# Optimization experiments

Measured on AMD Instinct MI355X. Metric: run time of the kernel, lower is better.

The kernel has to match this reference:

```python
import jax, jax.numpy as jnp
import numpy as np

N = 100000     # total points
PBS = 500      # point_batch_size (hard-coded in module)
K = 100        # num_neighbors
KP = 15        # num_kernel_points
EPS = 1e-5


def _bn(x, g, b, axes):
    # torch BatchNorm in training mode: batch stats, biased variance
    m = jnp.mean(x, axis=axes, keepdims=True)
    v = jnp.var(x, axis=axes, keepdims=True)
    return (x - m) / jnp.sqrt(v + EPS) * g + b


def setup_inputs() -> dict:
    key = jax.random.key(0)
    ks = jax.random.split(key, 16)
    rn = lambda k, sh, s=1.0: jax.random.normal(k, sh, jnp.float32) * s
    return {
        "pts": rn(ks[0], (N, 3)),
        "normal": rn(ks[1], (N, 3)),
        "kp_points": rn(ks[2], (KP, 3)),
        "kp_weights": rn(ks[3], (KP, 3, 128), 0.3),
        "kp_sigma": jnp.float32(1.0),
        "conv1_w": rn(ks[4], (1024, 128), 128 ** -0.5),
        "conv1_b": rn(ks[5], (1024,), 0.02),
        "bn1_g": jnp.ones((1024,), jnp.float32),
        "bn1_b": jnp.zeros((1024,), jnp.float32),
        "fc1_w": rn(ks[6], (512, 1024), 1024 ** -0.5),
        "fc1_b": rn(ks[7], (512,), 0.02),
        "bn4_g": jnp.ones((512,), jnp.float32),
        "bn4_b": jnp.zeros((512,), jnp.float32),
        "fc2_w": rn(ks[8], (256, 512), 512 ** -0.5),
        "fc2_b": rn(ks[9], (256,), 0.02),
        "bn5_g": jnp.ones((256,), jnp.float32),
        "bn5_b": jnp.zeros((256,), jnp.float32),
        "fc3_w": rn(ks[10], (3, 256), 256 ** -0.5),
        "fc3_b": rn(ks[11], (3,), 0.02),
        "index": jax.random.randint(ks[12], (PBS,), 0, N, jnp.int32),
    }


def reference(pts, normal, kp_points, kp_weights, kp_sigma,
              conv1_w, conv1_b, bn1_g, bn1_b,
              fc1_w, fc1_b, bn4_g, bn4_b,
              fc2_w, fc2_b, bn5_g, bn5_b,
              fc3_w, fc3_b, index):
    sel = pts[index]                                               # [B,3]
    # L-inf pairwise distance and kNN (topk of -dist, as in the torch code)
    dist = jnp.max(jnp.abs(sel[:, None, :] - pts[None, :, :]), axis=-1)  # [B,N]
    _, nbr = jax.lax.top_k(-dist, K)                               # [B,K]
    rel = pts[nbr] - sel[:, None, :]                               # [B,K,3]

    # KPConv: gaussian weights vs kernel points, per-kernel-point linear map
    d2 = jnp.sum((rel[:, :, None, :] - kp_points[None, None]) ** 2, axis=-1)  # [B,K,KP]
    w = jnp.exp(-0.5 * d2 / (kp_sigma ** 2))
    wf = rel[:, :, None, :] * w[..., None]                         # [B,K,KP,3]
    h = jax.nn.relu(jnp.einsum('bnkc,kco->bno', wf, kp_weights))   # [B,K,128]

    # 1x1 conv 128->1024, relu then BN over (batch, points) per channel
    h = jnp.einsum('bnc,oc->bno', h, conv1_w) + conv1_b            # [B,K,1024]
    h = _bn(jax.nn.relu(h), bn1_g, bn1_b, (0, 1))
    feat = jnp.max(h, axis=1)                                      # [B,1024]

    feat = _bn(jax.nn.relu(feat @ fc1_w.T + fc1_b), bn4_g, bn4_b, (0,))
    feat = _bn(jax.nn.relu(feat @ fc2_w.T + fc2_b), bn5_g, bn5_b, (0,))
    feat = feat @ fc3_w.T + fc3_b                                  # [B,3]
    return feat, normal[index]
```

## Files before the change

### kernel.cpp

```cpp
#include <hip/hip_runtime.h>
#include <hip/hip_fp16.h>

#define NPTS 100000
#define NB 500
#define KNN 100
#define KPN 15
#define C1 128
#define C2 1024
#define C3 512
#define C4 256

#define G 64
#define NCELLS (G * G * G)
#define GB 5.0f
#define GINVH ((float)G / (2.f * GB))
#define CAND_CAP 2048

typedef _Float16 half8 __attribute__((ext_vector_type(8)));
typedef float f32x4 __attribute__((ext_vector_type(4)));

__device__ __forceinline__ int cell_coord(float x) {
  int c = (int)floorf((x + GB) * GINVH);
  return min(max(c, 0), G - 1);
}
__device__ __forceinline__ int cell_of(float x, float y, float z) {
  return (cell_coord(x) << 12) | (cell_coord(y) << 6) | cell_coord(z);
}

__global__ __launch_bounds__(256) void prep_kernel(
    const float* __restrict__ pts, const float* __restrict__ normal,
    const int* __restrict__ index, const float* __restrict__ w1,
    const float* __restrict__ kpw, const float* __restrict__ fc1w,
    float* __restrict__ sel, float* __restrict__ out2,
    __half* __restrict__ wh, __half* __restrict__ kpwT_hi,
    __half* __restrict__ kpwT_lo, __half* __restrict__ fwhi,
    __half* __restrict__ fwlo, unsigned* __restrict__ cnt) {
  int i = blockIdx.x * 256 + threadIdx.x;
  if (i < NB) {
    int ix = index[i];
    sel[i * 3 + 0] = pts[3 * ix + 0];
    sel[i * 3 + 1] = pts[3 * ix + 1];
    sel[i * 3 + 2] = pts[3 * ix + 2];
    out2[i * 3 + 0] = normal[3 * ix + 0];
    out2[i * 3 + 1] = normal[3 * ix + 1];
    out2[i * 3 + 2] = normal[3 * ix + 2];
  }
  if (i < C2 * C1) wh[i] = __float2half(w1[i]);
  if (i < 128 * 64) {
    int o = i >> 6, j = i & 63;
    float v = (j < 45) ? kpw[j * 128 + o] : 0.f;
    __half hi = __float2half_rn(v);
    kpwT_hi[i] = hi;
    kpwT_lo[i] = __float2half_rn(v - __half2float(hi));
  }
  if (i < C3 * C2) {
    float v = fc1w[i];
    __half hi = __float2half_rn(v);
    fwhi[i] = hi;
    fwlo[i] = __float2half_rn(v - __half2float(hi));
  }
  if (i < NPTS)
    atomicAdd(&cnt[cell_of(pts[3 * i], pts[3 * i + 1], pts[3 * i + 2])], 1u);
}

__global__ __launch_bounds__(256) void grid_scan1_kernel(
    const unsigned* __restrict__ cnt, unsigned* __restrict__ cursor,
    unsigned* __restrict__ chunktot) {
  const int tid = threadIdx.x;
  int base = blockIdx.x * 1024 + tid * 4;
  unsigned c0 = cnt[base], c1 = cnt[base + 1], c2 = cnt[base + 2],
           c3 = cnt[base + 3];
  unsigned tot = c0 + c1 + c2 + c3;
  __shared__ unsigned sb[256];
  sb[tid] = tot;
  __syncthreads();
  for (int off = 1; off < 256; off <<= 1) {
    unsigned add = (tid >= off) ? sb[tid - off] : 0u;
    __syncthreads();
    sb[tid] += add;
    __syncthreads();
  }
  unsigned excl = sb[tid] - tot;
  cursor[base] = excl;
  cursor[base + 1] = excl + c0;
  cursor[base + 2] = excl + c0 + c1;
  cursor[base + 3] = excl + c0 + c1 + c2;
  if (tid == 255) chunktot[blockIdx.x] = sb[255];
}

__global__ __launch_bounds__(256) void grid_scan2_kernel(
    const unsigned* __restrict__ chunktot, unsigned* __restrict__ chunkoff) {
  const int tid = threadIdx.x;
  unsigned v = chunktot[tid];
  __shared__ unsigned sb[256];
  sb[tid] = v;
  __syncthreads();
  for (int off = 1; off < 256; off <<= 1) {
    unsigned add = (tid >= off) ? sb[tid - off] : 0u;
    __syncthreads();
    sb[tid] += add;
    __syncthreads();
  }
  chunkoff[tid] = sb[tid] - v;
}

__global__ __launch_bounds__(256) void grid_scan3_kernel(
    unsigned* __restrict__ cursor, const unsigned* __restrict__ chunkoff) {
  unsigned off = chunkoff[blockIdx.x];
  int base = blockIdx.x * 1024 + threadIdx.x * 4;
#pragma unroll
  for (int j = 0; j < 4; ++j) cursor[base + j] += off;
}

__global__ __launch_bounds__(256) void grid_scatter_kernel(
    const float* __restrict__ pts, unsigned* __restrict__ cursor,
    float4* __restrict__ sorted) {
  int i = blockIdx.x * 256 + threadIdx.x;
  if (i >= NPTS) return;
  float x = pts[3 * i], y = pts[3 * i + 1], z = pts[3 * i + 2];
  unsigned pos = atomicAdd(&cursor[cell_of(x, y, z)], 1u);
  sorted[pos] = make_float4(x, y, z, __int_as_float(i));
}

__device__ __forceinline__ unsigned linf_bits(float px, float py, float pz,
                                              float sx, float sy, float sz) {
  float dx = fabsf(px - sx), dy = fabsf(py - sy), dz = fabsf(pz - sz);
  return __float_as_uint(fmaxf(fmaxf(dx, dy), dz));
}

__global__ __launch_bounds__(256) void knn_kernel(
    const float4* __restrict__ sorted, const unsigned* __restrict__ cnt,
    const unsigned* __restrict__ cursor,
    const float* __restrict__ sel, int* __restrict__ nbr) {
  const int b = blockIdx.x;
  const int tid = threadIdx.x;
  __shared__ unsigned cbits[CAND_CAP];
  __shared__ int cidx[CAND_CAP];
  __shared__ unsigned hist[4096];
  __shared__ unsigned scanbuf[256];
  __shared__ int s_total, s_m, s_mc, s_chunk;
  __shared__ unsigned s_excl, s_bub;

  const float qx = sel[b * 3 + 0], qy = sel[b * 3 + 1], qz = sel[b * 3 + 2];
  const int qcx = cell_coord(qx), qcy = cell_coord(qy), qcz = cell_coord(qz);

  if (tid == 0) s_total = 0;
  __syncthreads();
  int s = 1;
  int pxlo = 1, pxhi = 0, pylo = 1, pyhi = 0, pzlo = 1, pzhi = 0;
  int xlo, xhi, ylo, yhi, zlo, zhi;
  for (;;) {
    xlo = max(qcx - s, 0); xhi = min(qcx + s, G - 1);
    ylo = max(qcy - s, 0); yhi = min(qcy + s, G - 1);
    zlo = max(qcz - s, 0); zhi = min(qcz + s, G - 1);
    int nx = xhi - xlo + 1, ny = yhi - ylo + 1, nz = zhi - zlo + 1;
    int ncell = nx * ny * nz;
    unsigned local = 0;
    for (int ci = tid; ci < ncell; ci += 256) {
      int cz = ci % nz;
      int r = ci / nz;
      int cy = r % ny;
      int cx = r / ny;
      int ax = xlo + cx, ay = ylo + cy, az = zlo + cz;
      if (ax >= pxlo && ax <= pxhi && ay >= pylo && ay <= pyhi &&
          az >= pzlo && az <= pzhi)
        continue;
      local += cnt[(ax << 12) | (ay << 6) | az];
    }
#pragma unroll
    for (int off = 32; off; off >>= 1) local += __shfl_down(local, off);
    if ((tid & 63) == 0) atomicAdd(&s_total, (int)local);
    __syncthreads();
    if (s_total >= KNN || (xlo == 0 && ylo == 0 && zlo == 0 && xhi == G - 1 &&
                           yhi == G - 1 && zhi == G - 1))
      break;
    pxlo = xlo; pxhi = xhi; pylo = ylo; pyhi = yhi; pzlo = zlo; pzhi = zhi;
    ++s;
    __syncthreads();
  }

  if (tid == 0) s_m = 0;
  __syncthreads();
  {
    int nx = xhi - xlo + 1, ny = yhi - ylo + 1, nz = zhi - zlo + 1;
    int ncell = nx * ny * nz;
    for (int ci = tid; ci < ncell; ci += 256) {
      int cz = ci % nz;
      int r = ci / nz;
      int cy = r % ny;
      int cx = r / ny;
      int cell = ((xlo + cx) << 12) | ((ylo + cy) << 6) | (zlo + cz);
      unsigned end = cursor[cell];
      unsigned beg = end - cnt[cell];
      int k = (int)(end - beg);
      if (k > 0) {
        int e0 = atomicAdd(&s_m, k);
        for (unsigned p = beg; p < end; ++p, ++e0) {
          if (e0 < CAND_CAP) {
            float4 f = sorted[p];
            cbits[e0] = linf_bits(f.x, f.y, f.z, qx, qy, qz);
            cidx[e0] = __float_as_int(f.w);
          }
        }
      }
    }
  }
  __syncthreads();
  int m = s_m < CAND_CAP ? s_m : CAND_CAP;

  for (int j = tid; j < 4096; j += 256) hist[j] = 0;
  __syncthreads();
  for (int e = tid; e < m; e += 256) atomicAdd(&hist[cbits[e] >> 19], 1u);
  __syncthreads();
  unsigned csum = 0;
  {
    int c0 = tid * 16;
#pragma unroll
    for (int j = 0; j < 16; ++j) csum += hist[c0 + j];
  }
  scanbuf[tid] = csum;
  __syncthreads();
  for (int off = 1; off < 256; off <<= 1) {
    unsigned add = (tid >= off) ? scanbuf[tid - off] : 0u;
    __syncthreads();
    scanbuf[tid] += add;
    __syncthreads();
  }
  {
    unsigned incl = scanbuf[tid], excl = incl - csum;
    if (excl < KNN && KNN <= incl) {
      s_chunk = tid;
      s_excl = excl;
    }
  }
  __syncthreads();
  if (tid == 0) {
    unsigned cum = s_excl;
    int bin = s_chunk * 16;
    while (cum + hist[bin] < KNN) {
      cum += hist[bin];
      ++bin;
    }
    s_bub = (unsigned)(bin + 1) << 19;
  }
  __syncthreads();

  const unsigned bub = s_bub;
  const float dub = __uint_as_float(bub);
  if (tid == 0) s_mc = 0;
  __syncthreads();
  {
    int xlo2 = min(max((int)floorf((qx - dub + GB) * GINVH), 0), G - 1);
    int xhi2 = min(max((int)floorf((qx + dub + GB) * GINVH), 0), G - 1);
    int ylo2 = min(max((int)floorf((qy - dub + GB) * GINVH), 0), G - 1);
    int yhi2 = min(max((int)floorf((qy + dub + GB) * GINVH), 0), G - 1);
    int zlo2 = min(max((int)floorf((qz - dub + GB) * GINVH), 0), G - 1);
    int zhi2 = min(max((int)floorf((qz + dub + GB) * GINVH), 0), G - 1);
    int nx = xhi2 - xlo2 + 1, ny = yhi2 - ylo2 + 1, nz = zhi2 - zlo2 + 1;
    int ncell = nx * ny * nz;
    for (int ci = tid; ci < ncell; ci += 256) {
      int cz = ci % nz;
      int r = ci / nz;
      int cy = r % ny;
      int cx = r / ny;
      int cell = ((xlo2 + cx) << 12) | ((ylo2 + cy) << 6) | (zlo2 + cz);
      unsigned end = cursor[cell];
      unsigned beg = end - cnt[cell];
      for (unsigned p = beg; p < end; ++p) {
        float4 f = sorted[p];
        unsigned bits = linf_bits(f.x, f.y, f.z, qx, qy, qz);
        if (bits < bub) {
          int e = atomicAdd(&s_mc, 1);
          if (e < CAND_CAP) {
            cbits[e] = bits;
            cidx[e] = __float_as_int(f.w);
          }
        }
      }
    }
  }
  __syncthreads();
  int mc = s_mc < CAND_CAP ? s_mc : CAND_CAP;

  for (int c = tid; c < mc; c += 256) {
    unsigned bc = cbits[c];
    int ic = cidx[c];
    int rank = 0;
    for (int j = 0; j < mc; ++j) {
      unsigned bj = cbits[j];
      rank += (bj < bc || (bj == bc && cidx[j] < ic)) ? 1 : 0;
    }
    if (rank < KNN) nbr[b * KNN + rank] = ic;
  }
}

__global__ __launch_bounds__(512, 2) void kpconv_conv1_kernel(
    const float* __restrict__ pts, const float* __restrict__ sel,
    const int* __restrict__ nbr, const float* __restrict__ kp_points,
    const __half* __restrict__ kpwT_hi, const __half* __restrict__ kpwT_lo,
    const float* __restrict__ kp_sigma, const __half* __restrict__ wh,
    const float* __restrict__ bias, float* __restrict__ featmax,
    float* __restrict__ featmin, float* __restrict__ bnsum,
    float* __restrict__ bnsq) {
  const int b = blockIdx.x;
  const int tid = threadIdx.x;
  const int wave = tid >> 6, lane = tid & 63;
  const int lr = lane & 15, quad = lane >> 4;

  __shared__ __align__(16) char smem[71168];
  __half* As_hi = (__half*)smem;
  __half* As_lo = As_hi + 112 * 72;
  __half* Bs_hi = As_lo + 112 * 72;
  __half* Bs_lo = Bs_hi + 128 * 72;
  float* rel = (float*)(Bs_lo + 128 * 72);
  float* kpp = rel + 100 * 4;
  __half* Hs = (__half*)smem;

  for (int i = tid; i < 128 * 8; i += 512) {
    int row = i >> 3, seg = i & 7;
    *(float4*)&Bs_hi[row * 72 + seg * 8] =
        *(const float4*)&kpwT_hi[row * 64 + seg * 8];
    *(float4*)&Bs_lo[row * 72 + seg * 8] =
        *(const float4*)&kpwT_lo[row * 64 + seg * 8];
  }
  {
    float4 z = make_float4(0.f, 0.f, 0.f, 0.f);
    for (int i = tid; i < 112 * 8; i += 512) {
      int row = i >> 3, seg = i & 7;
      *(float4*)&As_hi[row * 72 + seg * 8] = z;
      *(float4*)&As_lo[row * 72 + seg * 8] = z;
    }
  }
  if (tid < 45) kpp[tid] = kp_points[tid];
  if (tid < 100) {
    int idx = nbr[b * KNN + tid];
    rel[tid * 4 + 0] = pts[3 * idx + 0] - sel[b * 3 + 0];
    rel[tid * 4 + 1] = pts[3 * idx + 1] - sel[b * 3 + 1];
    rel[tid * 4 + 2] = pts[3 * idx + 2] - sel[b * 3 + 2];
  }
  __syncthreads();

  const float sg = kp_sigma[0];
  const float inv2s2 = -0.5f / (sg * sg);
  for (int i = tid; i < 100 * KPN; i += 512) {
    int k = i / KPN, p = i - k * KPN;
    float rx = rel[k * 4 + 0] - kpp[p * 3 + 0];
    float ry = rel[k * 4 + 1] - kpp[p * 3 + 1];
    float rz = rel[k * 4 + 2] - kpp[p * 3 + 2];
    float w = expf(inv2s2 * (rx * rx + ry * ry + rz * rz));
#pragma unroll
    for (int c = 0; c < 3; ++c) {
      float a = rel[k * 4 + c] * w;
      __half hi = __float2half_rn(a);
      As_hi[k * 72 + p * 3 + c] = hi;
      As_lo[k * 72 + p * 3 + c] = __float2half_rn(a - __half2float(hi));
    }
  }
  __syncthreads();

  f32x4 acc1[7];
#pragma unroll
  for (int m = 0; m < 7; ++m) acc1[m] = (f32x4)(0.f);
#pragma unroll
  for (int s = 0; s < 2; ++s) {
    int boff = (wave * 16 + lr) * 72 + s * 32 + quad * 8;
    half8 bhi = *(const half8*)&Bs_hi[boff];
    half8 blo = *(const half8*)&Bs_lo[boff];
#pragma unroll
    for (int m = 0; m < 7; ++m) {
      int aoff = (m * 16 + lr) * 72 + s * 32 + quad * 8;
      half8 ahi = *(const half8*)&As_hi[aoff];
      half8 alo = *(const half8*)&As_lo[aoff];
      acc1[m] = __builtin_amdgcn_mfma_f32_16x16x32_f16(ahi, bhi, acc1[m], 0, 0, 0);
      acc1[m] = __builtin_amdgcn_mfma_f32_16x16x32_f16(ahi, blo, acc1[m], 0, 0, 0);
      acc1[m] = __builtin_amdgcn_mfma_f32_16x16x32_f16(alo, bhi, acc1[m], 0, 0, 0);
    }
  }
  __syncthreads();

  {
    int col = wave * 16 + lr;
#pragma unroll
    for (int m = 0; m < 7; ++m)
#pragma unroll
      for (int r = 0; r < 4; ++r) {
        int row = m * 16 + quad * 4 + r;
        Hs[row * 136 + col] = __float2half_rn(fmaxf(acc1[m][r], 0.f));
      }
  }
  __syncthreads();

  half8 afr[4][7];
#pragma unroll
  for (int s = 0; s < 4; ++s)
#pragma unroll
    for (int m = 0; m < 7; ++m)
      afr[s][m] = *(const half8*)&Hs[(m * 16 + lr) * 136 + s * 32 + quad * 8];

  const int wrow = wave * 16 + lr;
  half8 bcur[4];
#pragma unroll
  for (int s = 0; s < 4; ++s)
    bcur[s] = *(const half8*)&wh[wrow * 128 + s * 32 + quad * 8];

  for (int c = 0; c < 8; ++c) {
    half8 bnxt[4];
    if (c + 1 < 8) {
#pragma unroll
      for (int s = 0; s < 4; ++s)
        bnxt[s] = *(const half8*)&wh[((c + 1) * 128 + wrow) * 128 + s * 32 +
                                     quad * 8];
    }

    f32x4 acc2[7];
#pragma unroll
    for (int m = 0; m < 7; ++m) acc2[m] = (f32x4)(0.f);
#pragma unroll
    for (int s = 0; s < 4; ++s)
#pragma unroll
      for (int m = 0; m < 7; ++m)
        acc2[m] = __builtin_amdgcn_mfma_f32_16x16x32_f16(afr[s][m], bcur[s],
                                                         acc2[m], 0, 0, 0);

    {
      int col = c * 128 + wrow;
      float bv = bias[col];
      float pmax = -1e30f, pmin = 1e30f, psum = 0.f, psq = 0.f;
#pragma unroll
      for (int m = 0; m < 7; ++m)
#pragma unroll
        for (int r = 0; r < 4; ++r) {
          int row = m * 16 + quad * 4 + r;
          if (row < 100) {
            float y = fmaxf(acc2[m][r] + bv, 0.f);
            pmax = fmaxf(pmax, y);
            pmin = fminf(pmin, y);
            psum += y;
            psq += y * y;
          }
        }
      pmax = fmaxf(pmax, __shfl_xor(pmax, 16));
      pmax = fmaxf(pmax, __shfl_xor(pmax, 32));
      pmin = fminf(pmin, __shfl_xor(pmin, 16));
      pmin = fminf(pmin, __shfl_xor(pmin, 32));
      psum += __shfl_xor(psum, 16);
      psum += __shfl_xor(psum, 32);
      psq += __shfl_xor(psq, 16);
      psq += __shfl_xor(psq, 32);
      if (quad == 0) {
        featmax[b * C2 + col] = pmax;
        featmin[b * C2 + col] = pmin;
        atomicAdd(&bnsum[col], psum);
        atomicAdd(&bnsq[col], psq);
      }
    }
#pragma unroll
    for (int s = 0; s < 4; ++s) bcur[s] = bnxt[s];
  }
}

__global__ __launch_bounds__(256) void bn1half_kernel(
    const float* __restrict__ featmax, const float* __restrict__ featmin,
    const float* __restrict__ bnsum, const float* __restrict__ bnsq,
    const float* __restrict__ g, const float* __restrict__ bb,
    __half* __restrict__ Xhi, __half* __restrict__ Xlo) {
  int idx = blockIdx.x * 256 + threadIdx.x;
  if (idx >= NB * C2) return;
  int o = idx & (C2 - 1);
  const float invn = 1.f / (float)(NB * KNN);
  float m = bnsum[o] * invn;
  float v = bnsq[o] * invn - m * m;
  float a = g[o] / sqrtf(v + 1e-5f);
  float x = (a >= 0.f) ? featmax[idx] : featmin[idx];
  float y = (x - m) * a + bb[o];
  __half hi = __float2half_rn(y);
  Xhi[idx] = hi;
  Xlo[idx] = __float2half_rn(y - __half2float(hi));
}

__global__ __launch_bounds__(256) void fc1_mfma_kernel(
    const __half* __restrict__ Xhi, const __half* __restrict__ Xlo,
    const __half* __restrict__ Whi, const __half* __restrict__ Wlo,
    const float* __restrict__ bias, float* __restrict__ yraw,
    float* __restrict__ s, float* __restrict__ sq) {
  const int r0 = blockIdx.x * 64;
  const int n0 = blockIdx.y * 64;
  const int tid = threadIdx.x;
  const int wave = tid >> 6, lane = tid & 63;
  const int lr = lane & 15, quad = lane >> 4;
  __shared__ __half Xs_hi[64 * 72], Xs_lo[64 * 72];
  __shared__ __half Ws_hi[64 * 72], Ws_lo[64 * 72];

  f32x4 acc[4];
#pragma unroll
  for (int m = 0; m < 4; ++m) acc[m] = (f32x4)(0.f);

  for (int kc = 0; kc < C2; kc += 64) {
    __syncthreads();
    for (int i = tid; i < 64 * 8; i += 256) {
      int row = i >> 3, seg = i & 7;
      int gr = r0 + row;
      float4 vhi = make_float4(0.f, 0.f, 0.f, 0.f), vlo = vhi;
      if (gr < NB) {
        vhi = *(const float4*)&Xhi[gr * C2 + kc + seg * 8];
        vlo = *(const float4*)&Xlo[gr * C2 + kc + seg * 8];
      }
      *(float4*)&Xs_hi[row * 72 + seg * 8] = vhi;
      *(float4*)&Xs_lo[row * 72 + seg * 8] = vlo;
      *(float4*)&Ws_hi[row * 72 + seg * 8] =
          *(const float4*)&Whi[(n0 + row) * C2 + kc + seg * 8];
      *(float4*)&Ws_lo[row * 72 + seg * 8] =
          *(const float4*)&Wlo[(n0 + row) * C2 + kc + seg * 8];
    }
    __syncthreads();

#pragma unroll
    for (int s2 = 0; s2 < 2; ++s2) {
      int boff = (wave * 16 + lr) * 72 + s2 * 32 + quad * 8;
      half8 bhi = *(const half8*)&Ws_hi[boff];
      half8 blo = *(const half8*)&Ws_lo[boff];
#pragma unroll
      for (int m = 0; m < 4; ++m) {
        int aoff = (m * 16 + lr) * 72 + s2 * 32 + quad * 8;
        half8 ahi = *(const half8*)&Xs_hi[aoff];
        half8 alo = *(const half8*)&Xs_lo[aoff];
        acc[m] = __builtin_amdgcn_mfma_f32_16x16x32_f16(ahi, bhi, acc[m], 0, 0, 0);
        acc[m] = __builtin_amdgcn_mfma_f32_16x16x32_f16(ahi, blo, acc[m], 0, 0, 0);
        acc[m] = __builtin_amdgcn_mfma_f32_16x16x32_f16(alo, bhi, acc[m], 0, 0, 0);
      }
    }
  }

  {
    int col = n0 + wave * 16 + lr;
    float bv = bias[col];
    float psum = 0.f, psq = 0.f;
#pragma unroll
    for (int m = 0; m < 4; ++m)
#pragma unroll
      for (int r = 0; r < 4; ++r) {
        int row = r0 + m * 16 + quad * 4 + r;
        if (row < NB) {
          float y = fmaxf(acc[m][r] + bv, 0.f);
          yraw[row * C3 + col] = y;
          psum += y;
          psq += y * y;
        }
      }
    psum += __shfl_xor(psum, 16);
    psum += __shfl_xor(psum, 32);
    psq += __shfl_xor(psq, 16);
    psq += __shfl_xor(psq, 32);
    if (quad == 0) {
      atomicAdd(&s[col], psum);
      atomicAdd(&sq[col], psq);
    }
  }
}

__global__ __launch_bounds__(256) void fc2_kernel(
    const float* __restrict__ x,
    const float* __restrict__ bnsum, const float* __restrict__ bnsq,
    const float* __restrict__ g, const float* __restrict__ bb,
    const float* __restrict__ w,
    const float* __restrict__ bias, float* __restrict__ yraw,
    float* __restrict__ s, float* __restrict__ sq) {
  const int r0 = blockIdx.x * 4;
  const int n0 = blockIdx.y * 64;
  const int tid = threadIdx.x;
  const int col = tid >> 2;
  const int row = tid & 3;
  __shared__ float xs[4][516];
  __shared__ float ws[64][132];
  __shared__ float amul[C3], badd[C3];
  const float invn = 1.f / (float)NB;
  for (int o = tid; o < C3; o += 256) {
    float m = bnsum[o] * invn;
    float v = bnsq[o] * invn - m * m;
    float a = g[o] / sqrtf(v + 1e-5f);
    amul[o] = a;
    badd[o] = bb[o] - m * a;
  }
  __syncthreads();
  for (int f = tid; f < C3; f += 256) {
    int rr = f >> 7, kq = (f & 127) * 4;
    float4 xv = *(const float4*)&x[(r0 + rr) * C3 + kq];
    float4 o4;
    o4.x = xv.x * amul[kq + 0] + badd[kq + 0];
    o4.y = xv.y * amul[kq + 1] + badd[kq + 1];
    o4.z = xv.z * amul[kq + 2] + badd[kq + 2];
    o4.w = xv.w * amul[kq + 3] + badd[kq + 3];
    *(float4*)&xs[rr][kq] = o4;
  }
  float acc = 0.f;
  for (int kc = 0; kc < C3; kc += 128) {
    __syncthreads();
#pragma unroll
    for (int i = 0; i < 8; ++i) {
      int f = tid + i * 256;
      int cr = f >> 5, kq = (f & 31) * 4;
      *(float4*)&ws[cr][kq] = *(const float4*)&w[(n0 + cr) * C3 + kc + kq];
    }
    __syncthreads();
    for (int kk = 0; kk < 128; kk += 4) {
      float4 xv = *(float4*)&xs[row][kc + kk];
      float4 wv = *(float4*)&ws[col][kk];
      acc += xv.x * wv.x + xv.y * wv.y + xv.z * wv.z + xv.w * wv.w;
    }
  }
  float y = fmaxf(acc + bias[n0 + col], 0.f);
  yraw[(r0 + row) * C4 + n0 + col] = y;
  float ys = y, y2 = y * y;
  ys += __shfl_xor(ys, 1); y2 += __shfl_xor(y2, 1);
  ys += __shfl_xor(ys, 2); y2 += __shfl_xor(y2, 2);
  if (row == 0) {
    atomicAdd(&s[n0 + col], ys);
    atomicAdd(&sq[n0 + col], y2);
  }
}

__global__ __launch_bounds__(256) void fc3_kernel(
    const float* __restrict__ x,
    const float* __restrict__ bnsum, const float* __restrict__ bnsq,
    const float* __restrict__ g, const float* __restrict__ bb,
    const float* __restrict__ w, const float* __restrict__ bias,
    float* __restrict__ out) {
  const int tid = threadIdx.x;
  __shared__ float pmul[C4], padd[C4];
  {
    const float invn = 1.f / (float)NB;
    float m = bnsum[tid] * invn;
    float v = bnsq[tid] * invn - m * m;
    float a = g[tid] / sqrtf(v + 1e-5f);
    pmul[tid] = a;
    padd[tid] = bb[tid] - m * a;
  }
  __syncthreads();
  int idx = blockIdx.x * 256 + tid;
  if (idx >= NB * 3) return;
  int b = idx / 3, o = idx % 3;
  float acc = 0.f;
  for (int k = 0; k < C4; ++k)
    acc += (x[b * C4 + k] * pmul[k] + padd[k]) * w[o * C4 + k];
  out[idx] = acc + bias[o];
}

extern "C" void kernel_launch(void* const* d_in, const int* in_sizes, int n_in,
                              void* d_out, int out_size, void* d_ws,
                              size_t ws_size, hipStream_t stream) {
  const float* pts = (const float*)d_in[0];
  const float* normal = (const float*)d_in[1];
  const float* kp_points = (const float*)d_in[2];
  const float* kp_weights = (const float*)d_in[3];
  const float* kp_sigma = (const float*)d_in[4];
  const float* conv1_w = (const float*)d_in[5];
  const float* conv1_b = (const float*)d_in[6];
  const float* bn1_g = (const float*)d_in[7];
  const float* bn1_b = (const float*)d_in[8];
  const float* fc1_w = (const float*)d_in[9];
  const float* fc1_b = (const float*)d_in[10];
  const float* bn4_g = (const float*)d_in[11];
  const float* bn4_b = (const float*)d_in[12];
  const float* fc2_w = (const float*)d_in[13];
  const float* fc2_b = (const float*)d_in[14];
  const float* bn5_g = (const float*)d_in[15];
  const float* bn5_b = (const float*)d_in[16];
  const float* fc3_w = (const float*)d_in[17];
  const float* fc3_b = (const float*)d_in[18];
  const int* index = (const int*)d_in[19];
  float* out = (float*)d_out;

  char* p = (char*)d_ws;
  auto carve = [&](size_t bytes) {
    void* r = (void*)p;
    p += (bytes + 255) & ~(size_t)255;
    return r;
  };
  float* sel = (float*)carve(NB * 3 * 4);
  int* nbr = (int*)carve(NB * KNN * 4);
  __half* wh = (__half*)carve((size_t)C2 * C1 * 2);
  __half* kpwT_hi = (__half*)carve((size_t)128 * 64 * 2);
  __half* kpwT_lo = (__half*)carve((size_t)128 * 64 * 2);
  __half* fwhi = (__half*)carve((size_t)C3 * C2 * 2);
  __half* fwlo = (__half*)carve((size_t)C3 * C2 * 2);
  __half* Xhi = (__half*)carve((size_t)NB * C2 * 2);
  __half* Xlo = (__half*)carve((size_t)NB * C2 * 2);
  float* featmax = (float*)carve(NB * C2 * 4);
  float* featmin = (float*)carve(NB * C2 * 4);
  float* f2raw = (float*)carve(NB * C3 * 4);
  float* f3raw = (float*)carve(NB * C4 * 4);
  float* stats = (float*)carve((2 * C2 + 2 * C3 + 2 * C4) * 4);
  float* bnsum = stats;
  float* bnsq = stats + C2;
  float* s4 = stats + 2 * C2;
  float* sq4 = s4 + C3;
  float* s5 = sq4 + C3;
  float* sq5 = s5 + C4;
  unsigned* cellcnt = (unsigned*)carve((size_t)NCELLS * 4);
  unsigned* cellcur = (unsigned*)carve((size_t)NCELLS * 4);
  unsigned* chunktot = (unsigned*)carve(256 * 4);
  unsigned* chunkoff = (unsigned*)carve(256 * 4);
  float4* sortedpts = (float4*)carve((size_t)NPTS * 16);

  hipMemsetAsync(stats, 0, (2 * C2 + 2 * C3 + 2 * C4) * 4, stream);
  hipMemsetAsync(cellcnt, 0, (size_t)NCELLS * 4, stream);

  prep_kernel<<<(C3 * C2 + 255) / 256, 256, 0, stream>>>(
      pts, normal, index, conv1_w, kp_weights, fc1_w, sel, out + NB * 3, wh,
      kpwT_hi, kpwT_lo, fwhi, fwlo, cellcnt);
  grid_scan1_kernel<<<256, 256, 0, stream>>>(cellcnt, cellcur, chunktot);
  grid_scan2_kernel<<<1, 256, 0, stream>>>(chunktot, chunkoff);
  grid_scan3_kernel<<<256, 256, 0, stream>>>(cellcur, chunkoff);
  grid_scatter_kernel<<<(NPTS + 255) / 256, 256, 0, stream>>>(pts, cellcur,
                                                              sortedpts);
  knn_kernel<<<NB, 256, 0, stream>>>(sortedpts, cellcnt, cellcur, sel, nbr);
  kpconv_conv1_kernel<<<NB, 512, 0, stream>>>(
      pts, sel, nbr, kp_points, kpwT_hi, kpwT_lo, kp_sigma, wh, conv1_b,
      featmax, featmin, bnsum, bnsq);
  bn1half_kernel<<<(NB * C2 + 255) / 256, 256, 0, stream>>>(
      featmax, featmin, bnsum, bnsq, bn1_g, bn1_b, Xhi, Xlo);
  fc1_mfma_kernel<<<dim3(8, 8), 256, 0, stream>>>(Xhi, Xlo, fwhi, fwlo, fc1_b,
                                                  f2raw, s4, sq4);
  fc2_kernel<<<dim3(125, C4 / 64), 256, 0, stream>>>(
      f2raw, s4, sq4, bn4_g, bn4_b, fc2_w, fc2_b, f3raw, s5, sq5);
  fc3_kernel<<<(NB * 3 + 255) / 256, 256, 0, stream>>>(
      f3raw, s5, sq5, bn5_g, bn5_b, fc3_w, fc3_b, out);
}
```

Measured before the change: 255.6 us.

## Use split-fp16 MFMA for fc2 and replace conv1 BN atomics with a reduction

The scalar fp32 fc2 kernel becomes an MFMA kernel that applies BN4 on the fly and splits activations and weights into fp16 hi/lo pairs, approximating fp32 accuracy with three MFMAs per tile. The fc2 weight split is done in the prep kernel. In the conv1 kernel, the per-block atomicAdds of BN statistics become per-row partial stores, summed by a new stats1 kernel. This is meant to cut fc2 compute time and remove atomic contention on 1024 columns from 500 blocks, at the cost of an extra launch and extra global traffic for the partial sums.

```diff
diff --git a/kernel.cpp b/kernel.cpp
--- a/kernel.cpp
+++ b/kernel.cpp
@@ -31,10 +31,12 @@
     const float* __restrict__ pts, const float* __restrict__ normal,
     const int* __restrict__ index, const float* __restrict__ w1,
     const float* __restrict__ kpw, const float* __restrict__ fc1w,
-    float* __restrict__ sel, float* __restrict__ out2,
-    __half* __restrict__ wh, __half* __restrict__ kpwT_hi,
-    __half* __restrict__ kpwT_lo, __half* __restrict__ fwhi,
-    __half* __restrict__ fwlo, unsigned* __restrict__ cnt) {
+    const float* __restrict__ fc2w, float* __restrict__ sel,
+    float* __restrict__ out2, __half* __restrict__ wh,
+    __half* __restrict__ kpwT_hi, __half* __restrict__ kpwT_lo,
+    __half* __restrict__ fwhi, __half* __restrict__ fwlo,
+    __half* __restrict__ f2whi, __half* __restrict__ f2wlo,
+    unsigned* __restrict__ cnt) {
   int i = blockIdx.x * 256 + threadIdx.x;
   if (i < NB) {
     int ix = index[i];
@@ -58,6 +60,12 @@
     __half hi = __float2half_rn(v);
     fwhi[i] = hi;
     fwlo[i] = __float2half_rn(v - __half2float(hi));
+  }
+  if (i < C4 * C3) {
+    float v = fc2w[i];
+    __half hi = __float2half_rn(v);
+    f2whi[i] = hi;
+    f2wlo[i] = __float2half_rn(v - __half2float(hi));
   }
   if (i < NPTS)
     atomicAdd(&cnt[cell_of(pts[3 * i], pts[3 * i + 1], pts[3 * i + 2])], 1u);
@@ -300,8 +308,8 @@
     const __half* __restrict__ kpwT_hi, const __half* __restrict__ kpwT_lo,
     const float* __restrict__ kp_sigma, const __half* __restrict__ wh,
     const float* __restrict__ bias, float* __restrict__ featmax,
-    float* __restrict__ featmin, float* __restrict__ bnsum,
-    float* __restrict__ bnsq) {
+    float* __restrict__ featmin, float* __restrict__ featsum,
+    float* __restrict__ featsq) {
   const int b = blockIdx.x;
   const int tid = threadIdx.x;
   const int wave = tid >> 6, lane = tid & 63;
@@ -450,13 +458,27 @@
       if (quad == 0) {
         featmax[b * C2 + col] = pmax;
         featmin[b * C2 + col] = pmin;
-        atomicAdd(&bnsum[col], psum);
-        atomicAdd(&bnsq[col], psq);
+        featsum[b * C2 + col] = psum;
+        featsq[b * C2 + col] = psq;
       }
     }
 #pragma unroll
     for (int s = 0; s < 4; ++s) bcur[s] = bnxt[s];
   }
+}
+
+__global__ __launch_bounds__(256) void stats1_kernel(
+    const float* __restrict__ featsum, const float* __restrict__ featsq,
+    float* __restrict__ bnsum, float* __restrict__ bnsq) {
+  int col = blockIdx.x * 256 + threadIdx.x;
+  int r0 = blockIdx.y * 50;
+  float s = 0.f, q = 0.f;
+  for (int r = r0; r < r0 + 50; ++r) {
+    s += featsum[r * C2 + col];
+    q += featsq[r * C2 + col];
+  }
+  atomicAdd(&bnsum[col], s);
+  atomicAdd(&bnsq[col], q);
 }
 
 __global__ __launch_bounds__(256) void bn1half_kernel(
@@ -558,64 +580,112 @@
   }
 }
 
-__global__ __launch_bounds__(256) void fc2_kernel(
+__global__ __launch_bounds__(256) void fc2_mfma_kernel(
     const float* __restrict__ x,
-    const float* __restrict__ bnsum, const float* __restrict__ bnsq,
+    const float* __restrict__ bnsum4, const float* __restrict__ bnsq4,
     const float* __restrict__ g, const float* __restrict__ bb,
-    const float* __restrict__ w,
+    const __half* __restrict__ Whi, const __half* __restrict__ Wlo,
     const float* __restrict__ bias, float* __restrict__ yraw,
     float* __restrict__ s, float* __restrict__ sq) {
-  const int r0 = blockIdx.x * 4;
+  const int r0 = blockIdx.x * 64;
   const int n0 = blockIdx.y * 64;
   const int tid = threadIdx.x;
-  const int col = tid >> 2;
-  const int row = tid & 3;
-  __shared__ float xs[4][516];
-  __shared__ float ws[64][132];
+  const int wave = tid >> 6, lane = tid & 63;
+  const int lr = lane & 15, quad = lane >> 4;
+  __shared__ __half Xs_hi[64 * 72], Xs_lo[64 * 72];
+  __shared__ __half Ws_hi[64 * 72], Ws_lo[64 * 72];
   __shared__ float amul[C3], badd[C3];
-  const float invn = 1.f / (float)NB;
-  for (int o = tid; o < C3; o += 256) {
-    float m = bnsum[o] * invn;
-    float v = bnsq[o] * invn - m * m;
-    float a = g[o] / sqrtf(v + 1e-5f);
-    amul[o] = a;
-    badd[o] = bb[o] - m * a;
-  }
-  __syncthreads();
-  for (int f = tid; f < C3; f += 256) {
-    int rr = f >> 7, kq = (f & 127) * 4;
-    float4 xv = *(const float4*)&x[(r0 + rr) * C3 + kq];
-    float4 o4;
-    o4.x = xv.x * amul[kq + 0] + badd[kq + 0];
-    o4.y = xv.y * amul[kq + 1] + badd[kq + 1];
-    o4.z = xv.z * amul[kq + 2] + badd[kq + 2];
-    o4.w = xv.w * amul[kq + 3] + badd[kq + 3];
-    *(float4*)&xs[rr][kq] = o4;
-  }
-  float acc = 0.f;
-  for (int kc = 0; kc < C3; kc += 128) {
-    __syncthreads();
-#pragma unroll
-    for (int i = 0; i < 8; ++i) {
-      int f = tid + i * 256;
-      int cr = f >> 5, kq = (f & 31) * 4;
-      *(float4*)&ws[cr][kq] = *(const float4*)&w[(n0 + cr) * C3 + kc + kq];
-    }
-    __syncthreads();
-    for (int kk = 0; kk < 128; kk += 4) {
-      float4 xv = *(float4*)&xs[row][kc + kk];
-      float4 wv = *(float4*)&ws[col][kk];
-      acc += xv.x * wv.x + xv.y * wv.y + xv.z * wv.z + xv.w * wv.w;
-    }
-  }
-  float y = fmaxf(acc + bias[n0 + col], 0.f);
-  yraw[(r0 + row) * C4 + n0 + col] = y;
-  float ys = y, y2 = y * y;
-  ys += __shfl_xor(ys, 1); y2 += __shfl_xor(y2, 1);
-  ys += __shfl_xor(ys, 2); y2 += __shfl_xor(y2, 2);
-  if (row == 0) {
-    atomicAdd(&s[n0 + col], ys);
-    atomicAdd(&sq[n0 + col], y2);
+
+  {
+    const float invn = 1.f / (float)NB;
+    for (int o = tid; o < C3; o += 256) {
+      float m = bnsum4[o] * invn;
+      float v = bnsq4[o] * invn - m * m;
+      float a = g[o] / sqrtf(v + 1e-5f);
+      amul[o] = a;
+      badd[o] = bb[o] - m * a;
+    }
+  }
+
+  f32x4 acc[4];
+#pragma unroll
+  for (int m = 0; m < 4; ++m) acc[m] = (f32x4)(0.f);
+
+  for (int kc = 0; kc < C3; kc += 64) {
+    __syncthreads();
+    for (int i = tid; i < 64 * 8; i += 256) {
+      int row = i >> 3, seg = i & 7;
+      int gr = r0 + row;
+      __half hbuf[8], lbuf[8];
+      if (gr < NB) {
+        float4 a0 = *(const float4*)&x[gr * C3 + kc + seg * 8];
+        float4 a1 = *(const float4*)&x[gr * C3 + kc + seg * 8 + 4];
+        float vals[8] = {a0.x, a0.y, a0.z, a0.w, a1.x, a1.y, a1.z, a1.w};
+#pragma unroll
+        for (int j = 0; j < 8; ++j) {
+          int o = kc + seg * 8 + j;
+          float y = vals[j] * amul[o] + badd[o];
+          __half hi = __float2half_rn(y);
+          hbuf[j] = hi;
+          lbuf[j] = __float2half_rn(y - __half2float(hi));
+        }
+      } else {
+#pragma unroll
+        for (int j = 0; j < 8; ++j) {
+          hbuf[j] = __float2half_rn(0.f);
+          lbuf[j] = __float2half_rn(0.f);
+        }
+      }
+      *(float4*)&Xs_hi[row * 72 + seg * 8] = *(float4*)hbuf;
+      *(float4*)&Xs_lo[row * 72 + seg * 8] = *(float4*)lbuf;
+      *(float4*)&Ws_hi[row * 72 + seg * 8] =
+          *(const float4*)&Whi[(n0 + row) * C3 + kc + seg * 8];
+      *(float4*)&Ws_lo[row * 72 + seg * 8] =
+          *(const float4*)&Wlo[(n0 + row) * C3 + kc + seg * 8];
+    }
+    __syncthreads();
+
+#pragma unroll
+    for (int s2 = 0; s2 < 2; ++s2) {
+      int boff = (wave * 16 + lr) * 72 + s2 * 32 + quad * 8;
+      half8 bhi = *(const half8*)&Ws_hi[boff];
+      half8 blo = *(const half8*)&Ws_lo[boff];
+#pragma unroll
+      for (int m = 0; m < 4; ++m) {
+        int aoff = (m * 16 + lr) * 72 + s2 * 32 + quad * 8;
+        half8 ahi = *(const half8*)&Xs_hi[aoff];
+        half8 alo = *(const half8*)&Xs_lo[aoff];
+        acc[m] = __builtin_amdgcn_mfma_f32_16x16x32_f16(ahi, bhi, acc[m], 0, 0, 0);
+        acc[m] = __builtin_amdgcn_mfma_f32_16x16x32_f16(ahi, blo, acc[m], 0, 0, 0);
+        acc[m] = __builtin_amdgcn_mfma_f32_16x16x32_f16(alo, bhi, acc[m], 0, 0, 0);
+      }
+    }
+  }
+
+  {
+    int col = n0 + wave * 16 + lr;
+    float bv = bias[col];
+    float psum = 0.f, psq = 0.f;
+#pragma unroll
+    for (int m = 0; m < 4; ++m)
+#pragma unroll
+      for (int r = 0; r < 4; ++r) {
+        int row = r0 + m * 16 + quad * 4 + r;
+        if (row < NB) {
+          float y = fmaxf(acc[m][r] + bv, 0.f);
+          yraw[row * C4 + col] = y;
+          psum += y;
+          psq += y * y;
+        }
+      }
+    psum += __shfl_xor(psum, 16);
+    psum += __shfl_xor(psum, 32);
+    psq += __shfl_xor(psq, 16);
+    psq += __shfl_xor(psq, 32);
+    if (quad == 0) {
+      atomicAdd(&s[col], psum);
+      atomicAdd(&sq[col], psq);
+    }
   }
 }
 
@@ -683,10 +753,14 @@
   __half* kpwT_lo = (__half*)carve((size_t)128 * 64 * 2);
   __half* fwhi = (__half*)carve((size_t)C3 * C2 * 2);
   __half* fwlo = (__half*)carve((size_t)C3 * C2 * 2);
+  __half* f2whi = (__half*)carve((size_t)C4 * C3 * 2);
+  __half* f2wlo = (__half*)carve((size_t)C4 * C3 * 2);
   __half* Xhi = (__half*)carve((size_t)NB * C2 * 2);
   __half* Xlo = (__half*)carve((size_t)NB * C2 * 2);
   float* featmax = (float*)carve(NB * C2 * 4);
   float* featmin = (float*)carve(NB * C2 * 4);
+  float* featsum = (float*)carve(NB * C2 * 4);
+  float* featsq = (float*)carve(NB * C2 * 4);
   float* f2raw = (float*)carve(NB * C3 * 4);
   float* f3raw = (float*)carve(NB * C4 * 4);
   float* stats = (float*)carve((2 * C2 + 2 * C3 + 2 * C4) * 4);
@@ -706,8 +780,8 @@
   hipMemsetAsync(cellcnt, 0, (size_t)NCELLS * 4, stream);
 
   prep_kernel<<<(C3 * C2 + 255) / 256, 256, 0, stream>>>(
-      pts, normal, index, conv1_w, kp_weights, fc1_w, sel, out + NB * 3, wh,
-      kpwT_hi, kpwT_lo, fwhi, fwlo, cellcnt);
+      pts, normal, index, conv1_w, kp_weights, fc1_w, fc2_w, sel,
+      out + NB * 3, wh, kpwT_hi, kpwT_lo, fwhi, fwlo, f2whi, f2wlo, cellcnt);
   grid_scan1_kernel<<<256, 256, 0, stream>>>(cellcnt, cellcur, chunktot);
   grid_scan2_kernel<<<1, 256, 0, stream>>>(chunktot, chunkoff);
   grid_scan3_kernel<<<256, 256, 0, stream>>>(cellcur, chunkoff);
@@ -716,13 +790,15 @@
   knn_kernel<<<NB, 256, 0, stream>>>(sortedpts, cellcnt, cellcur, sel, nbr);
   kpconv_conv1_kernel<<<NB, 512, 0, stream>>>(
       pts, sel, nbr, kp_points, kpwT_hi, kpwT_lo, kp_sigma, wh, conv1_b,
-      featmax, featmin, bnsum, bnsq);
+      featmax, featmin, featsum, featsq);
+  stats1_kernel<<<dim3(4, 10), 256, 0, stream>>>(featsum, featsq, bnsum,
+                                                 bnsq);
   bn1half_kernel<<<(NB * C2 + 255) / 256, 256, 0, stream>>>(
       featmax, featmin, bnsum, bnsq, bn1_g, bn1_b, Xhi, Xlo);
   fc1_mfma_kernel<<<dim3(8, 8), 256, 0, stream>>>(Xhi, Xlo, fwhi, fwlo, fc1_b,
                                                   f2raw, s4, sq4);
-  fc2_kernel<<<dim3(125, C4 / 64), 256, 0, stream>>>(
-      f2raw, s4, sq4, bn4_g, bn4_b, fc2_w, fc2_b, f3raw, s5, sq5);
+  fc2_mfma_kernel<<<dim3(8, 4), 256, 0, stream>>>(
+      f2raw, s4, sq4, bn4_g, bn4_b, f2whi, f2wlo, fc2_b, f3raw, s5, sq5);
   fc3_kernel<<<(NB * 3 + 255) / 256, 256, 0, stream>>>(
       f3raw, s5, sq5, bn5_g, bn5_b, fc3_w, fc3_b, out);
 }
```

New measurement: 261.9 us. 2.5% more time.
